# Optimization experiments

Hardware: AMD Instinct MI355X
Metric: run time of the kernel (lower is better)

Reference implementation:

```python
import jax, jax.numpy as jnp
import numpy as np

WORLD_SIZE = 8  # number of ring participants / sequence blocks
NEG_INF = jnp.float32(-jnp.inf)


def setup_inputs() -> dict:
    key = jax.random.key(0)
    kq, kk, kv = jax.random.split(key, 3)
    B, S, H, D = 2, 8192, 16, 64
    return {
        "query": jax.random.normal(kq, (B, S, H, D), dtype=jnp.float32),
        "key": jax.random.normal(kk, (B, S, H, D), dtype=jnp.float32),
        "value": jax.random.normal(kv, (B, S, H, D), dtype=jnp.float32),
    }


def reference(query, key, value):
    """Ring attention: blockwise QK^T + per-block softmax with running
    (max, sum, acc) online-softmax merge across ring steps. Causal.
    query/key/value: [B, S, H, D]. Output: [B, S, H, D].
    Mathematically equal to exact causal attention, computed with the
    block/LSE-merge structure of the ring algorithm (never materializes
    the full [S, S] score matrix).
    """
    W = WORLD_SIZE
    B, S, H, D = query.shape
    Bs = S // W  # local block (per-rank) sequence length
    scale = 1.0 / np.sqrt(D)

    # [W, B, Bs, H, D] blocks along the sequence axis
    qb = query.reshape(B, W, Bs, H, D).transpose(1, 0, 2, 3, 4)
    kb = key.reshape(B, W, Bs, H, D).transpose(1, 0, 2, 3, 4)
    vb = value.reshape(B, W, Bs, H, D).transpose(1, 0, 2, 3, 4)

    diag_mask = jnp.arange(Bs)[:, None] >= jnp.arange(Bs)[None, :]  # [Bs, Bs]

    outs = []
    for r in range(W):  # query block owned by rank r
        q = qb[r]  # [B, Bs, H, D]
        m = jnp.full((B, H, Bs), NEG_INF, dtype=jnp.float32)   # running row max
        l = jnp.zeros((B, H, Bs), dtype=jnp.float32)           # running sum-exp
        acc = jnp.zeros((B, H, Bs, D), dtype=jnp.float32)      # running numerator
        for j in range(r + 1):  # causal: fully-masked future kv blocks skipped
            s = jnp.einsum('bqhd,bkhd->bhqk', q, kb[j]).astype(jnp.float32) * scale
            if j == r:  # diagonal block: per-element causal mask
                s = jnp.where(diag_mask, s, NEG_INF)
            m_new = jnp.maximum(m, s.max(axis=-1))
            p = jnp.exp(s - m_new[..., None])                   # [B, H, Bs, Bs]
            alpha = jnp.exp(m - m_new)
            l = l * alpha + p.sum(axis=-1)
            acc = acc * alpha[..., None] + jnp.einsum(
                'bhqk,bkhd->bhqd', p, vb[j].astype(jnp.float32))
            m = m_new
        out_r = (acc / l[..., None]).astype(query.dtype)  # [B, H, Bs, D]
        outs.append(out_r.transpose(0, 2, 1, 3))          # -> [B, Bs, H, D]
    return jnp.concatenate(outs, axis=1)  # [B, S, H, D]
```

## Files before the change

kernel.cpp:

```cpp
#include <hip/hip_runtime.h>
#include <hip/hip_bf16.h>

typedef __attribute__((ext_vector_type(8))) short short8;
typedef __attribute__((ext_vector_type(4))) short short4_t;
typedef __attribute__((ext_vector_type(4))) float float4_t;
typedef __attribute__((ext_vector_type(16))) float floatx16;

constexpr int S_LEN = 8192;
constexpr int NHEAD = 16;
constexpr int DHEAD = 64;
constexpr int RS    = NHEAD * DHEAD;
constexpr int BK    = 64;
constexpr int QW    = 32;
constexpr int NWAVE = 4;
constexpr int QTILE = QW * NWAVE;
constexpr int PADK  = 72;

__device__ __forceinline__ unsigned int cvt2bf(float lo, float hi) {
  __hip_bfloat162 h2 = __float22bfloat162_rn(make_float2(lo, hi));
  unsigned int u;
  __builtin_memcpy(&u, &h2, 4);
  return u;
}

__device__ __forceinline__ float fast_exp2(float x) {
#if __has_builtin(__builtin_amdgcn_exp2f)
  return __builtin_amdgcn_exp2f(x);
#else
  return exp2f(x);
#endif
}

__global__ __launch_bounds__(256, 4)
void fattn_kernel(const float* __restrict__ Qg,
                  const float* __restrict__ Kg,
                  const float* __restrict__ Vg,
                  float* __restrict__ Og)
{
  __shared__ __align__(16) unsigned short Kl[BK * PADK];
  __shared__ __align__(16) unsigned short Vl[DHEAD * PADK];

  const int tid  = threadIdx.x;
  const int wave = tid >> 6;
  const int lane = tid & 63;
  const int m31  = lane & 31;
  const int h    = lane >> 5;

  const int blk = blockIdx.x;
  const int bh  = blk & 31;
  const int qt  = 63 - (blk >> 5);
  const int b   = bh >> 4;
  const int h_  = bh & 15;

  const int q0  = qt * QTILE;
  const int qw0 = q0 + wave * QW;

  const size_t base = ((size_t)b * S_LEN * NHEAD + h_) * DHEAD;
  const float* Qp = Qg + base;
  const float* Kp = Kg + base;
  const float* Vp = Vg + base;
  float*       Op = Og + base;

  const float qs = 0.125f * 1.44269504088896340736f;
  short8 qf[4];
#pragma unroll
  for (int c = 0; c < 4; ++c) {
    const float* p = Qp + (size_t)(qw0 + m31) * RS + 16 * c + 8 * h;
    float4_t a = *(const float4_t*)p;
    float4_t d = *(const float4_t*)(p + 4);
    union { short8 s; unsigned int u[4]; } r;
    r.u[0] = cvt2bf(a[0] * qs, a[1] * qs);
    r.u[1] = cvt2bf(a[2] * qs, a[3] * qs);
    r.u[2] = cvt2bf(d[0] * qs, d[1] * qs);
    r.u[3] = cvt2bf(d[2] * qs, d[3] * qs);
    qf[c] = r.s;
  }

  floatx16 acc[2];
#pragma unroll
  for (int md = 0; md < 2; ++md)
#pragma unroll
    for (int r = 0; r < 16; ++r) acc[md][r] = 0.f;

  float l_run = 0.f;

  const int sr  = tid >> 4;
  const int sc4 = (tid & 15) * 4;
  const int vd  = tid & 63;
  const int vg0 = tid >> 6;

  const int kend = q0 + QTILE;
  for (int k0 = 0; k0 < kend; k0 += BK) {
    {
      const float* kp = Kp + (size_t)(k0 + sr) * RS + sc4;
#pragma unroll
      for (int ps = 0; ps < 4; ++ps) {
        float4_t v = *(const float4_t*)(kp + (size_t)ps * 16 * RS);
        uint2 pk = make_uint2(cvt2bf(v[0], v[1]), cvt2bf(v[2], v[3]));
        *(uint2*)&Kl[(sr + ps * 16) * PADK + sc4] = pk;
      }
#pragma unroll
      for (int p = 0; p < 2; ++p) {
        const int vg = vg0 + 4 * p;
        const float* vp = Vp + (size_t)(k0 + 8 * vg) * RS + vd;
        float x0 = vp[0 * RS], x1 = vp[1 * RS], x2 = vp[2 * RS], x3 = vp[3 * RS];
        float x4 = vp[4 * RS], x5 = vp[5 * RS], x6 = vp[6 * RS], x7 = vp[7 * RS];
        uint4 pk = make_uint4(cvt2bf(x0, x1), cvt2bf(x2, x3),
                              cvt2bf(x4, x5), cvt2bf(x6, x7));
        *(uint4*)&Vl[vd * PADK + 8 * vg] = pk;
      }
    }
    __syncthreads();

    if (k0 < qw0 + QW) {
      floatx16 ST[2];
#pragma unroll
      for (int kvm2 = 0; kvm2 < 2; ++kvm2) {
#pragma unroll
        for (int r = 0; r < 16; ++r) ST[kvm2][r] = 0.f;
#pragma unroll
        for (int c = 0; c < 4; ++c) {
          short8 aK = *(const short8*)&Kl[(32 * kvm2 + m31) * PADK + 16 * c + 8 * h];
          ST[kvm2] = __builtin_amdgcn_mfma_f32_32x32x16_bf16(aK, qf[c], ST[kvm2], 0, 0, 0);
        }
      }

      if (k0 + BK > qw0) {
        const int qpos = qw0 + m31;
#pragma unroll
        for (int kvm2 = 0; kvm2 < 2; ++kvm2)
#pragma unroll
          for (int r = 0; r < 16; ++r) {
            int kpos = k0 + 32 * kvm2 + (r & 3) + 8 * (r >> 2) + 4 * h;
            if (kpos > qpos) ST[kvm2][r] = -__builtin_inff();
          }
      }

      unsigned int D[2][8];
      float ps0 = 0.f, ps1 = 0.f;
#pragma unroll
      for (int kvm2 = 0; kvm2 < 2; ++kvm2)
#pragma unroll
        for (int i = 0; i < 8; ++i) {
          float e0 = fast_exp2(ST[kvm2][2 * i]);
          float e1 = fast_exp2(ST[kvm2][2 * i + 1]);
          D[kvm2][i] = cvt2bf(e0, e1);
          if (i & 1) ps1 += e0 + e1; else ps0 += e0 + e1;
        }
      l_run += ps0 + ps1;

#pragma unroll
      for (int t = 0; t < 4; ++t) {
        const int u  = t & 1;
        const int kb = 32 * (t >> 1) + 16 * u;
        union { short8 s; unsigned int u32[4]; } bf;
        bf.u32[0] = D[t >> 1][4 * u + 0];
        bf.u32[1] = D[t >> 1][4 * u + 1];
        bf.u32[2] = D[t >> 1][4 * u + 2];
        bf.u32[3] = D[t >> 1][4 * u + 3];
#pragma unroll
        for (int md = 0; md < 2; ++md) {
          const unsigned short* vr = &Vl[(32 * md + m31) * PADK + kb + 4 * h];
          short4_t lo = *(const short4_t*)(vr);
          short4_t hi = *(const short4_t*)(vr + 8);
          short8 aV = __builtin_shufflevector(lo, hi, 0, 1, 2, 3, 4, 5, 6, 7);
          acc[md] = __builtin_amdgcn_mfma_f32_32x32x16_bf16(aV, bf.s, acc[md], 0, 0, 0);
        }
      }
    }
    __syncthreads();
  }

  float l = l_run + __shfl_xor(l_run, 32);
  float inv = 1.0f / l;
  float* op = Op + (size_t)(qw0 + m31) * RS;
#pragma unroll
  for (int md = 0; md < 2; ++md)
#pragma unroll
    for (int g = 0; g < 4; ++g) {
      float4_t o;
#pragma unroll
      for (int j = 0; j < 4; ++j) o[j] = acc[md][4 * g + j] * inv;
      *(float4_t*)(op + 32 * md + 8 * g + 4 * h) = o;
    }
}

extern "C" void kernel_launch(void* const* d_in, const int* in_sizes, int n_in,
                              void* d_out, int out_size, void* d_ws, size_t ws_size,
                              hipStream_t stream) {
  const float* q = (const float*)d_in[0];
  const float* k = (const float*)d_in[1];
  const float* v = (const float*)d_in[2];
  float* o = (float*)d_out;
  fattn_kernel<<<dim3(2048), dim3(256), 0, stream>>>(q, k, v, o);
}
```

Measured before the change: 559.3 us.

## Pre-convert K/V to swizzled bf16 workspace and double-buffer via global_load_lds

Adds two prep kernels that convert K to bf16 in a per-head contiguous, XOR-swizzled layout and transpose V into bf16 tiles. The attention kernel then streams these tiles straight into LDS with global_load_lds, double-buffered so the next block's load overlaps compute, with one barrier per iteration. This removes the repeated fp32 loads, conversions and strided V gathers that every query tile did on every KV block. The cost is two extra launches and workspace traffic, and the old path is kept as a fallback when no workspace is given.

```diff
diff --git a/kernel.cpp b/kernel.cpp
--- a/kernel.cpp
+++ b/kernel.cpp
@@ -14,7 +14,11 @@
 constexpr int QW    = 32;
 constexpr int NWAVE = 4;
 constexpr int QTILE = QW * NWAVE;
+constexpr int BH    = 32;
 constexpr int PADK  = 72;
+
+constexpr size_t KB_ELEMS  = (size_t)BH * S_LEN * DHEAD;
+constexpr size_t WS_NEEDED = 2 * KB_ELEMS * sizeof(unsigned short);
 
 __device__ __forceinline__ unsigned int cvt2bf(float lo, float hi) {
   __hip_bfloat162 h2 = __float22bfloat162_rn(make_float2(lo, hi));
@@ -31,14 +35,80 @@
 #endif
 }
 
+__device__ __forceinline__ void gload_lds16(const unsigned short* g, unsigned short* l) {
+  __builtin_amdgcn_global_load_lds(
+      (const __attribute__((address_space(1))) unsigned int*)g,
+      (__attribute__((address_space(3))) unsigned int*)l, 16, 0, 0);
+}
+
+__global__ __launch_bounds__(256)
+void kprep_kernel(const float* __restrict__ Kg, unsigned short* __restrict__ Kb)
+{
+  const int bs = blockIdx.x;
+  const int b  = bs >> 13;
+  const int s  = bs & 8191;
+  const int t  = threadIdx.x;
+  const int hh = t >> 4;
+  const int q4 = t & 15;
+
+  const float* src = Kg + ((size_t)(b * S_LEN + s) * NHEAD + hh) * DHEAD + 4 * q4;
+  float4_t v = *(const float4_t*)src;
+  uint2 pk = make_uint2(cvt2bf(v[0], v[1]), cvt2bf(v[2], v[3]));
+
+  const int slot = (q4 >> 1) ^ (s & 7);
+  const int half = q4 & 1;
+  unsigned short* dst = Kb + ((size_t)((b * NHEAD + hh) * S_LEN + s)) * DHEAD
+                           + slot * 8 + half * 4;
+  *(uint2*)dst = pk;
+}
+
+__global__ __launch_bounds__(256)
+void vprep_kernel(const float* __restrict__ Vg, unsigned short* __restrict__ Vb)
+{
+  __shared__ float Lf[64 * 65];
+
+  const int blk  = blockIdx.x;
+  const int bh   = blk & 31;
+  const int tile = blk >> 5;
+  const int b    = bh >> 4;
+  const int hh   = bh & 15;
+  const int t    = threadIdx.x;
+  const int s0   = tile * 64;
+
+  const int kvr = t >> 4;
+  const int d4  = (t & 15) * 4;
+#pragma unroll
+  for (int p = 0; p < 4; ++p) {
+    int kv = kvr + 16 * p;
+    float4_t x = *(const float4_t*)&Vg[((size_t)(b * S_LEN + s0 + kv) * NHEAD + hh) * DHEAD + d4];
+#pragma unroll
+    for (int j = 0; j < 4; ++j) Lf[(d4 + j) * 65 + kv] = x[j];
+  }
+  __syncthreads();
+
+  const int d2 = t >> 3;
+  const int sp = t & 7;
+#pragma unroll
+  for (int i = 0; i < 2; ++i) {
+    int dd    = d2 + 32 * i;
+    int s_log = sp ^ (dd & 7);
+    int kb    = 16 * (s_log >> 1) + 4 * (s_log & 1);
+    const float* r = &Lf[dd * 65];
+    uint4 pk = make_uint4(cvt2bf(r[kb + 0], r[kb + 1]),
+                          cvt2bf(r[kb + 2], r[kb + 3]),
+                          cvt2bf(r[kb + 8], r[kb + 9]),
+                          cvt2bf(r[kb + 10], r[kb + 11]));
+    *(uint4*)&Vb[(((size_t)(bh * 128 + tile)) * 64 + dd) * 64 + sp * 8] = pk;
+  }
+}
+
 __global__ __launch_bounds__(256, 4)
-void fattn_kernel(const float* __restrict__ Qg,
-                  const float* __restrict__ Kg,
-                  const float* __restrict__ Vg,
-                  float* __restrict__ Og)
+void fattn_fast(const float* __restrict__ Qg,
+                const unsigned short* __restrict__ Kb,
+                const unsigned short* __restrict__ Vb,
+                float* __restrict__ Og)
 {
-  __shared__ __align__(16) unsigned short Kl[BK * PADK];
-  __shared__ __align__(16) unsigned short Vl[DHEAD * PADK];
+  __shared__ __align__(16) unsigned short SM[2][2][4096];
 
   const int tid  = threadIdx.x;
   const int wave = tid >> 6;
@@ -57,9 +127,10 @@
 
   const size_t base = ((size_t)b * S_LEN * NHEAD + h_) * DHEAD;
   const float* Qp = Qg + base;
-  const float* Kp = Kg + base;
-  const float* Vp = Vg + base;
   float*       Op = Og + base;
+
+  const unsigned short* kgp = Kb + (size_t)bh * (S_LEN * DHEAD) + wave * 512 + lane * 8;
+  const unsigned short* vgp = Vb + (size_t)bh * (S_LEN * DHEAD) + wave * 512 + lane * 8;
 
   const float qs = 0.125f * 1.44269504088896340736f;
   short8 qf[4];
@@ -84,6 +155,158 @@
 
   float l_run = 0.f;
 
+  const int s7 = m31 & 7;
+  int off[2][4];
+#pragma unroll
+  for (int x = 0; x < 2; ++x)
+#pragma unroll
+    for (int c = 0; c < 4; ++c)
+      off[x][c] = (32 * x + m31) * 64 + (((2 * c + h) ^ s7) << 3);
+
+  const int kend = q0 + QTILE;
+
+  gload_lds16(kgp,        &SM[0][0][wave * 512]);
+  gload_lds16(kgp + 2048, &SM[0][0][wave * 512 + 2048]);
+  gload_lds16(vgp,        &SM[0][1][wave * 512]);
+  gload_lds16(vgp + 2048, &SM[0][1][wave * 512 + 2048]);
+
+  int cur = 0;
+  for (int k0 = 0; k0 < kend; k0 += BK) {
+    asm volatile("s_waitcnt vmcnt(0)" ::: "memory");
+    __syncthreads();
+
+    if (k0 + BK < kend) {
+      const unsigned short* kp = kgp + (size_t)(k0 + BK) * 64;
+      const unsigned short* vp = vgp + (size_t)(k0 + BK) * 64;
+      const int nb = cur ^ 1;
+      gload_lds16(kp,        &SM[nb][0][wave * 512]);
+      gload_lds16(kp + 2048, &SM[nb][0][wave * 512 + 2048]);
+      gload_lds16(vp,        &SM[nb][1][wave * 512]);
+      gload_lds16(vp + 2048, &SM[nb][1][wave * 512 + 2048]);
+    }
+
+    if (k0 < qw0 + QW) {
+      floatx16 ST[2];
+#pragma unroll
+      for (int kvm2 = 0; kvm2 < 2; ++kvm2) {
+#pragma unroll
+        for (int r = 0; r < 16; ++r) ST[kvm2][r] = 0.f;
+#pragma unroll
+        for (int c = 0; c < 4; ++c) {
+          short8 aK = *(const short8*)&SM[cur][0][off[kvm2][c]];
+          ST[kvm2] = __builtin_amdgcn_mfma_f32_32x32x16_bf16(aK, qf[c], ST[kvm2], 0, 0, 0);
+        }
+      }
+
+      if (k0 + BK > qw0) {
+        const int qpos = qw0 + m31;
+#pragma unroll
+        for (int kvm2 = 0; kvm2 < 2; ++kvm2)
+#pragma unroll
+          for (int r = 0; r < 16; ++r) {
+            int kpos = k0 + 32 * kvm2 + (r & 3) + 8 * (r >> 2) + 4 * h;
+            if (kpos > qpos) ST[kvm2][r] = -__builtin_inff();
+          }
+      }
+
+      unsigned int D[2][8];
+      float ps0 = 0.f, ps1 = 0.f;
+#pragma unroll
+      for (int kvm2 = 0; kvm2 < 2; ++kvm2)
+#pragma unroll
+        for (int i = 0; i < 8; ++i) {
+          float e0 = fast_exp2(ST[kvm2][2 * i]);
+          float e1 = fast_exp2(ST[kvm2][2 * i + 1]);
+          D[kvm2][i] = cvt2bf(e0, e1);
+          if (i & 1) ps1 += e0 + e1; else ps0 += e0 + e1;
+        }
+      l_run += ps0 + ps1;
+
+#pragma unroll
+      for (int t = 0; t < 4; ++t) {
+        const int u = t & 1;
+        union { short8 s; unsigned int u32[4]; } bf;
+        bf.u32[0] = D[t >> 1][4 * u + 0];
+        bf.u32[1] = D[t >> 1][4 * u + 1];
+        bf.u32[2] = D[t >> 1][4 * u + 2];
+        bf.u32[3] = D[t >> 1][4 * u + 3];
+#pragma unroll
+        for (int md = 0; md < 2; ++md) {
+          short8 aV = *(const short8*)&SM[cur][1][off[md][t]];
+          acc[md] = __builtin_amdgcn_mfma_f32_32x32x16_bf16(aV, bf.s, acc[md], 0, 0, 0);
+        }
+      }
+    }
+    cur ^= 1;
+  }
+
+  float l = l_run + __shfl_xor(l_run, 32);
+  float inv = 1.0f / l;
+  float* op = Op + (size_t)(qw0 + m31) * RS;
+#pragma unroll
+  for (int md = 0; md < 2; ++md)
+#pragma unroll
+    for (int g = 0; g < 4; ++g) {
+      float4_t o;
+#pragma unroll
+      for (int j = 0; j < 4; ++j) o[j] = acc[md][4 * g + j] * inv;
+      *(float4_t*)(op + 32 * md + 8 * g + 4 * h) = o;
+    }
+}
+
+__global__ __launch_bounds__(256, 4)
+void fattn_legacy(const float* __restrict__ Qg,
+                  const float* __restrict__ Kg,
+                  const float* __restrict__ Vg,
+                  float* __restrict__ Og)
+{
+  __shared__ __align__(16) unsigned short Kl[BK * PADK];
+  __shared__ __align__(16) unsigned short Vl[DHEAD * PADK];
+
+  const int tid  = threadIdx.x;
+  const int wave = tid >> 6;
+  const int lane = tid & 63;
+  const int m31  = lane & 31;
+  const int h    = lane >> 5;
+
+  const int blk = blockIdx.x;
+  const int bh  = blk & 31;
+  const int qt  = 63 - (blk >> 5);
+  const int b   = bh >> 4;
+  const int h_  = bh & 15;
+
+  const int q0  = qt * QTILE;
+  const int qw0 = q0 + wave * QW;
+
+  const size_t base = ((size_t)b * S_LEN * NHEAD + h_) * DHEAD;
+  const float* Qp = Qg + base;
+  const float* Kp = Kg + base;
+  const float* Vp = Vg + base;
+  float*       Op = Og + base;
+
+  const float qs = 0.125f * 1.44269504088896340736f;
+  short8 qf[4];
+#pragma unroll
+  for (int c = 0; c < 4; ++c) {
+    const float* p = Qp + (size_t)(qw0 + m31) * RS + 16 * c + 8 * h;
+    float4_t a = *(const float4_t*)p;
+    float4_t d = *(const float4_t*)(p + 4);
+    union { short8 s; unsigned int u[4]; } r;
+    r.u[0] = cvt2bf(a[0] * qs, a[1] * qs);
+    r.u[1] = cvt2bf(a[2] * qs, a[3] * qs);
+    r.u[2] = cvt2bf(d[0] * qs, d[1] * qs);
+    r.u[3] = cvt2bf(d[2] * qs, d[3] * qs);
+    qf[c] = r.s;
+  }
+
+  floatx16 acc[2];
+#pragma unroll
+  for (int md = 0; md < 2; ++md)
+#pragma unroll
+    for (int r = 0; r < 16; ++r) acc[md][r] = 0.f;
+
+  float l_run = 0.f;
+
   const int sr  = tid >> 4;
   const int sc4 = (tid & 15) * 4;
   const int vd  = tid & 63;
@@ -192,5 +415,14 @@
   const float* k = (const float*)d_in[1];
   const float* v = (const float*)d_in[2];
   float* o = (float*)d_out;
-  fattn_kernel<<<dim3(2048), dim3(256), 0, stream>>>(q, k, v, o);
-}
+
+  if (d_ws != nullptr && ws_size >= WS_NEEDED) {
+    unsigned short* Kb = (unsigned short*)d_ws;
+    unsigned short* Vb = Kb + KB_ELEMS;
+    kprep_kernel<<<dim3(16384), dim3(256), 0, stream>>>(k, Kb);
+    vprep_kernel<<<dim3(4096),  dim3(256), 0, stream>>>(v, Vb);
+    fattn_fast  <<<dim3(2048),  dim3(256), 0, stream>>>(q, Kb, Vb, o);
+  } else {
+    fattn_legacy<<<dim3(2048), dim3(256), 0, stream>>>(q, k, v, o);
+  }
+}
```

Result: faster. 488.7 us (-12.6%).
